# Kernel tuning notes

Measured on AMD Instinct MI355X. Metric: run time of the kernel, lower is better.

The kernel has to match this reference:

```python
import math
import jax, jax.numpy as jnp
import numpy as np

L, W, H, T, B = 12, 1024, 16, 1024, 2
CH = W // H  # per-head channels
SCALE = 1.0 / math.sqrt(math.sqrt(CH))
STD = 0.25 * math.sqrt(1.0 / W)  # init_scale * sqrt(1/width)


def setup_inputs() -> dict:
    key = jax.random.key(0)
    ks = jax.random.split(key, 8)
    x = jax.random.normal(ks[0], (B, T, W), dtype=jnp.float32)
    qkv_w = jax.random.normal(ks[1], (L, W, 3 * W), dtype=jnp.float32) * STD
    qkv_b = jnp.zeros((L, 3 * W), jnp.float32)
    proj_w = jax.random.normal(ks[2], (L, W, W), dtype=jnp.float32) * STD
    proj_b = jnp.zeros((L, W), jnp.float32)
    ln1_g = jnp.ones((L, W), jnp.float32)
    ln1_b = jnp.zeros((L, W), jnp.float32)
    ln2_g = jnp.ones((L, W), jnp.float32)
    ln2_b = jnp.zeros((L, W), jnp.float32)
    fc_w = jax.random.normal(ks[3], (L, W, 4 * W), dtype=jnp.float32) * STD
    fc_b = jnp.zeros((L, 4 * W), jnp.float32)
    fc2_w = jax.random.normal(ks[4], (L, 4 * W, W), dtype=jnp.float32) * STD
    fc2_b = jnp.zeros((L, W), jnp.float32)
    return dict(x=x, qkv_w=qkv_w, qkv_b=qkv_b, proj_w=proj_w, proj_b=proj_b,
                ln1_g=ln1_g, ln1_b=ln1_b, ln2_g=ln2_g, ln2_b=ln2_b,
                fc_w=fc_w, fc_b=fc_b, fc2_w=fc2_w, fc2_b=fc2_b)


def _ln(x, g, b, eps=1e-5):
    mu = jnp.mean(x, axis=-1, keepdims=True)
    var = jnp.mean(jnp.square(x - mu), axis=-1, keepdims=True)
    return (x - mu) * jax.lax.rsqrt(var + eps) * g + b


def _attn(h, w_qkv, b_qkv, w_p, b_p):
    bs, t, w = h.shape
    qkv = (h @ w_qkv + b_qkv).reshape(bs, t, H, 3 * CH)
    q, k, v = jnp.split(qkv, 3, axis=-1)  # each [bs, t, H, CH]
    # double-sqrt scaling as in QKVMultiheadAttention
    wts = jnp.einsum('bthc,bshc->bhts', q * SCALE, k * SCALE)
    wts = jax.nn.softmax(wts.astype(jnp.float32), axis=-1).astype(h.dtype)
    o = jnp.einsum('bhts,bshc->bthc', wts, v).reshape(bs, t, w)
    return o @ w_p + b_p


def reference(x, qkv_w, qkv_b, proj_w, proj_b, ln1_g, ln1_b, ln2_g, ln2_b,
              fc_w, fc_b, fc2_w, fc2_b):
    def step(h, p):
        wq, bq, wp, bp, g1, b1, g2, b2, wf, bf, w2, b2m = p
        h = h + _attn(_ln(h, g1, b1), wq, bq, wp, bp)
        z = _ln(h, g2, b2)
        h = h + (jax.nn.gelu(z @ wf + bf, approximate=False) @ w2 + b2m)
        return h, None
    params = (qkv_w, qkv_b, proj_w, proj_b, ln1_g, ln1_b, ln2_g, ln2_b,
              fc_w, fc_b, fc2_w, fc2_b)
    out, _ = jax.lax.scan(step, x, params)
    return out
```

## Files before the change

kernel.cpp:

```cpp
#include <hip/hip_runtime.h>
#include <hip/hip_bf16.h>
#include <math.h>

typedef __bf16 bf16;
typedef __bf16 bf16x8 __attribute__((ext_vector_type(8)));
typedef __bf16 bf16x4 __attribute__((ext_vector_type(4)));
typedef float  f32x4  __attribute__((ext_vector_type(4)));

#define DEV __device__ __forceinline__

DEV void lds_load16(const void* g, void* l) {
  __builtin_amdgcn_global_load_lds(
      (__attribute__((address_space(1))) unsigned int*)g,
      (__attribute__((address_space(3))) unsigned int*)l, 16, 0, 0);
}

DEV f32x4 mfma16(bf16x8 a, bf16x8 b, f32x4 c) {
  return __builtin_amdgcn_mfma_f32_16x16x32_bf16(a, b, c, 0, 0, 0);
}

__global__ __launch_bounds__(256) void transpose_cvt(
    const float* __restrict__ in0, bf16* __restrict__ out0, int R, int C) {
  __shared__ float t[32][33];
  size_t zo = (size_t)blockIdx.z * R * C;
  const float* in = in0 + zo;
  bf16* out = out0 + zo;
  int tx = threadIdx.x, ty = threadIdx.y;
  int c0 = blockIdx.x * 32, r0 = blockIdx.y * 32;
#pragma unroll
  for (int i = 0; i < 4; i++)
    t[ty + i * 8][tx] = in[(size_t)(r0 + ty + i * 8) * C + c0 + tx];
  __syncthreads();
#pragma unroll
  for (int i = 0; i < 4; i++)
    out[(size_t)(c0 + ty + i * 8) * R + r0 + tx] = (bf16)t[tx][ty + i * 8];
}

__global__ __launch_bounds__(256) void ln_fwd(
    const float* __restrict__ x, const float* __restrict__ gw,
    const float* __restrict__ bw, bf16* __restrict__ y,
    float* __restrict__ hout) {
  int row = blockIdx.x, tid = threadIdx.x;
  const float4 v = ((const float4*)(x + (size_t)row * 1024))[tid];
  if (hout) ((float4*)(hout + (size_t)row * 1024))[tid] = v;
  float s  = v.x + v.y + v.z + v.w;
  float s2 = v.x * v.x + v.y * v.y + v.z * v.z + v.w * v.w;
#pragma unroll
  for (int o = 1; o < 64; o <<= 1) {
    s  += __shfl_xor(s, o);
    s2 += __shfl_xor(s2, o);
  }
  __shared__ float ps[4], ps2[4];
  int wv = tid >> 6;
  if ((tid & 63) == 0) { ps[wv] = s; ps2[wv] = s2; }
  __syncthreads();
  s  = ps[0] + ps[1] + ps[2] + ps[3];
  s2 = ps2[0] + ps2[1] + ps2[2] + ps2[3];
  float mu  = s * (1.f / 1024.f);
  float var = s2 * (1.f / 1024.f) - mu * mu;
  float rs  = rsqrtf(var + 1e-5f);
  float4 gv = ((const float4*)gw)[tid];
  float4 bv = ((const float4*)bw)[tid];
  bf16x4 o4;
  o4[0] = (bf16)((v.x - mu) * rs * gv.x + bv.x);
  o4[1] = (bf16)((v.y - mu) * rs * gv.y + bv.y);
  o4[2] = (bf16)((v.z - mu) * rs * gv.z + bv.z);
  o4[3] = (bf16)((v.w - mu) * rs * gv.w + bv.w);
  *(bf16x4*)(y + (size_t)row * 1024 + tid * 4) = o4;
}

__global__ __launch_bounds__(256) void reduce_ln(
    const float* __restrict__ parts, int nparts, const float* __restrict__ bias,
    float* __restrict__ h, const float* __restrict__ gw,
    const float* __restrict__ bw, bf16* __restrict__ y) {
  const int row = blockIdx.x, tid = threadIdx.x;
  const size_t MN = (size_t)gridDim.x * 1024;
  const size_t rb = (size_t)row * 256;
  float4 s = ((const float4*)parts)[rb + tid];
  for (int p = 1; p < nparts; p++) {
    float4 v = ((const float4*)(parts + (size_t)p * MN))[rb + tid];
    s.x += v.x; s.y += v.y; s.z += v.z; s.w += v.w;
  }
  const float4 bb = ((const float4*)bias)[tid];
  float4 r = ((float4*)h)[rb + tid];
  r.x += s.x + bb.x; r.y += s.y + bb.y; r.z += s.z + bb.z; r.w += s.w + bb.w;
  ((float4*)h)[rb + tid] = r;
  if (gw == nullptr) return;
  float sm  = r.x + r.y + r.z + r.w;
  float sm2 = r.x * r.x + r.y * r.y + r.z * r.z + r.w * r.w;
#pragma unroll
  for (int o = 1; o < 64; o <<= 1) {
    sm  += __shfl_xor(sm, o);
    sm2 += __shfl_xor(sm2, o);
  }
  __shared__ float ps[4], ps2[4];
  int wv = tid >> 6;
  if ((tid & 63) == 0) { ps[wv] = sm; ps2[wv] = sm2; }
  __syncthreads();
  sm  = ps[0] + ps[1] + ps[2] + ps[3];
  sm2 = ps2[0] + ps2[1] + ps2[2] + ps2[3];
  float mu  = sm * (1.f / 1024.f);
  float var = sm2 * (1.f / 1024.f) - mu * mu;
  float rs  = rsqrtf(var + 1e-5f);
  float4 gv = ((const float4*)gw)[tid];
  float4 bv = ((const float4*)bw)[tid];
  bf16x4 o4;
  o4[0] = (bf16)((r.x - mu) * rs * gv.x + bv.x);
  o4[1] = (bf16)((r.y - mu) * rs * gv.y + bv.y);
  o4[2] = (bf16)((r.z - mu) * rs * gv.z + bv.z);
  o4[3] = (bf16)((r.w - mu) * rs * gv.w + bv.w);
  *(bf16x4*)(y + (size_t)row * 1024 + tid * 4) = o4;
}

template <int EPI>
__global__ __launch_bounds__(512, 2) void gemm8p(
    const bf16* __restrict__ A, const bf16* __restrict__ Bt,
    const float* __restrict__ bias, float* __restrict__ outf,
    bf16* __restrict__ outb, int M, int N, int K, int kcount) {
  __shared__ __align__(16) char lds[3 * 49152];
  const int tid = threadIdx.x, wv = tid >> 6, lane = tid & 63;
  const int g = lane >> 4, lr = lane & 15;
  const int wr = wv >> 2, wc = wv & 3;
  const int bn = blockIdx.x, bm = blockIdx.y;
  const int kbegin = blockIdx.z * kcount;
  const bf16* Ab = A + (size_t)bm * 128 * K + kbegin;
  const bf16* Bb = Bt + (size_t)bn * 256 * K + kbegin;
  const int nt = kcount >> 6;

  f32x4 acc[4][4] = {};

  auto stageA = [&](int t) {
    char* dst = lds + (t % 3) * 49152;
    int k0 = t * 64;
#pragma unroll
    for (int c = 0; c < 2; c++) {
      int off = c * 8192 + tid * 16;
      int row = off >> 7, cb = off & 127;
      int cbs = cb ^ ((row & 7) << 4);
      lds_load16((const char*)(Ab + (size_t)row * K + k0) + cbs, dst + off);
    }
  };
  auto stageB = [&](int t, int half) {
    char* dst = lds + (t % 3) * 49152 + 16384 + half * 16384;
    int k0 = t * 64;
#pragma unroll
    for (int c = 0; c < 2; c++) {
      int off = c * 8192 + tid * 16;
      int row = (off >> 7) + half * 128, cb = off & 127;
      int cbs = cb ^ ((row & 7) << 4);
      lds_load16((const char*)(Bb + (size_t)row * K + k0) + cbs, dst + off);
    }
  };
  auto ldA = [&](int t, int m, int kk) -> bf16x8 {
    const char* base = lds + (t % 3) * 49152;
    int row = wr * 64 + m * 16 + lr;
    int col = (kk * 64 + g * 16) ^ ((row & 7) << 4);
    return *(const bf16x8*)(base + row * 128 + col);
  };
  auto ldB = [&](int t, int n, int kk) -> bf16x8 {
    const char* base = lds + (t % 3) * 49152 + 16384;
    int row = wc * 64 + n * 16 + lr;
    int col = (kk * 64 + g * 16) ^ ((row & 7) << 4);
    return *(const bf16x8*)(base + row * 128 + col);
  };

  stageA(0); stageB(0, 0); stageB(0, 1);
  if (nt > 1) {
    stageA(1); stageB(1, 0); stageB(1, 1);
    asm volatile("s_waitcnt vmcnt(6)" ::: "memory");
  } else {
    asm volatile("s_waitcnt vmcnt(0)" ::: "memory");
  }
  __builtin_amdgcn_s_barrier();

  bf16x8 a[4][2], b[4][2];
  for (int t = 0; t < nt; ++t) {
#pragma unroll
    for (int m = 0; m < 4; m++)
#pragma unroll
      for (int kk = 0; kk < 2; kk++) a[m][kk] = ldA(t, m, kk);
#pragma unroll
    for (int n = 0; n < 2; n++)
#pragma unroll
      for (int kk = 0; kk < 2; kk++) b[n][kk] = ldB(t, n, kk);
    if (t + 2 < nt) { stageA(t + 2); stageB(t + 2, 0); }
    __builtin_amdgcn_s_barrier();
    asm volatile("s_waitcnt lgkmcnt(0)" ::: "memory");
    __builtin_amdgcn_sched_barrier(0);
    __builtin_amdgcn_s_setprio(1);
#pragma unroll
    for (int m = 0; m < 4; m++)
#pragma unroll
      for (int n = 0; n < 2; n++)
#pragma unroll
        for (int kk = 0; kk < 2; kk++)
          acc[m][n] = mfma16(a[m][kk], b[n][kk], acc[m][n]);
    __builtin_amdgcn_s_setprio(0);
    __builtin_amdgcn_s_barrier();
#pragma unroll
    for (int n = 2; n < 4; n++)
#pragma unroll
      for (int kk = 0; kk < 2; kk++) b[n][kk] = ldB(t, n, kk);
    if (t + 2 < nt) {
      stageB(t + 2, 1);
      asm volatile("s_waitcnt vmcnt(6)" ::: "memory");
    } else if (t + 1 < nt) {
      asm volatile("s_waitcnt vmcnt(0)" ::: "memory");
    }
    __builtin_amdgcn_s_barrier();
    asm volatile("s_waitcnt lgkmcnt(0)" ::: "memory");
    __builtin_amdgcn_sched_barrier(0);
    __builtin_amdgcn_s_setprio(1);
#pragma unroll
    for (int m = 0; m < 4; m++)
#pragma unroll
      for (int n = 2; n < 4; n++)
#pragma unroll
        for (int kk = 0; kk < 2; kk++)
          acc[m][n] = mfma16(a[m][kk], b[n][kk], acc[m][n]);
    __builtin_amdgcn_s_setprio(0);
    __builtin_amdgcn_s_barrier();
  }

  float* po = (EPI == 3) ? outf + (size_t)blockIdx.z * M * N : outf;
#pragma unroll
  for (int m = 0; m < 4; m++) {
#pragma unroll
    for (int n = 0; n < 4; n++) {
      int col = bn * 256 + wc * 64 + n * 16 + lr;
      float bv = (EPI == 3) ? 0.f : bias[col];
#pragma unroll
      for (int r = 0; r < 4; r++) {
        int row = bm * 128 + wr * 64 + m * 16 + g * 4 + r;
        size_t idx = (size_t)row * N + col;
        float v = acc[m][n][r] + bv;
        if (EPI == 0) {
          outb[idx] = (bf16)v;
        } else if (EPI == 2) {
          outb[idx] = (bf16)(0.5f * v * (1.f + erff(v * 0.70710678118f)));
        } else {
          po[idx] = v;
        }
      }
    }
  }
}

__global__ __launch_bounds__(256) void attn_fwd(
    const bf16* __restrict__ qkv, bf16* __restrict__ outp) {
  __shared__ __align__(16) bf16 Kls[128 * 64];
  __shared__ __align__(16) bf16 Vt[64 * 128];
  __shared__ __align__(16) bf16 Pls[4 * 16 * 128];
  const int tid = threadIdx.x, wv = tid >> 6, lane = tid & 63;
  const int g = lane >> 4, lr = lane & 15;
  const int bh = blockIdx.y, bb = bh >> 4, hh = bh & 15;
  const int q0 = blockIdx.x * 64;
  const bf16* base = qkv + (size_t)bb * 1024 * 3072;
  const int qc = hh * 192, kc = qc + 64, vc = qc + 128;

  bf16x8 aq[2];
  {
    int row = q0 + wv * 16 + lr;
#pragma unroll
    for (int kk = 0; kk < 2; kk++) {
      bf16x8 v = *(const bf16x8*)(base + (size_t)row * 3072 + qc + kk * 32 + g * 8);
#pragma unroll
      for (int j = 0; j < 8; j++) v[j] = (bf16)((float)v[j] * 0.1803368801f);
      aq[kk] = v;
    }
  }

  f32x4 o[4] = {};
  float rm[4], rl[4];
#pragma unroll
  for (int r = 0; r < 4; r++) { rm[r] = -1e30f; rl[r] = 0.f; }

  for (int s0 = 0; s0 < 1024; s0 += 128) {
#pragma unroll
    for (int c = 0; c < 4; c++) {
      int off = wv * 4096 + c * 1024 + lane * 16;
      int s = off >> 7, cb = off & 127;
      int cbs = cb ^ ((s & 7) << 4);
      lds_load16((const char*)(base + (size_t)(s0 + s) * 3072 + kc) + cbs,
                 (char*)Kls + off);
    }
#pragma unroll
    for (int it = 0; it < 2; it++) {
      int idx = it * 256 + tid;
      int s = (idx >> 3) * 2, c0i = (idx & 7) * 8;
      bf16x8 v0 = *(const bf16x8*)(base + (size_t)(s0 + s) * 3072 + vc + c0i);
      bf16x8 v1 = *(const bf16x8*)(base + (size_t)(s0 + s + 1) * 3072 + vc + c0i);
#pragma unroll
      for (int j = 0; j < 8; j++) {
        int c = c0i + j;
        unsigned int pk = (unsigned int)__builtin_bit_cast(unsigned short, v0[j]) |
                          ((unsigned int)__builtin_bit_cast(unsigned short, v1[j]) << 16);
        *(unsigned int*)((char*)Vt + c * 256 + ((s * 2) ^ ((c & 7) << 4))) = pk;
      }
    }
    __syncthreads();
    f32x4 sa[8] = {};
#pragma unroll
    for (int kk = 0; kk < 2; kk++) {
#pragma unroll
      for (int n = 0; n < 8; n++) {
        int srow = n * 16 + lr;
        int cbyte = (kk * 32 + g * 8) * 2;
        bf16x8 kb = *(const bf16x8*)((char*)Kls + srow * 128 +
                                     (cbyte ^ ((srow & 7) << 4)));
        sa[n] = mfma16(aq[kk], kb, sa[n]);
      }
    }
    float al[4];
#pragma unroll
    for (int r = 0; r < 4; r++) {
      float tm = -1e30f;
#pragma unroll
      for (int n = 0; n < 8; n++) tm = fmaxf(tm, sa[n][r]);
      tm = fmaxf(tm, __shfl_xor(tm, 1));
      tm = fmaxf(tm, __shfl_xor(tm, 2));
      tm = fmaxf(tm, __shfl_xor(tm, 4));
      tm = fmaxf(tm, __shfl_xor(tm, 8));
      float nm = fmaxf(rm[r], tm);
      al[r] = exp2f(rm[r] - nm);
      rm[r] = nm;
    }
    float psum[4] = {0.f, 0.f, 0.f, 0.f};
#pragma unroll
    for (int n = 0; n < 8; n++) {
#pragma unroll
      for (int r = 0; r < 4; r++) {
        float p = exp2f(sa[n][r] - rm[r]);
        psum[r] += p;
        int rw = g * 4 + r;
        int sb = (n * 16 + lr) * 2;
        *(bf16*)((char*)Pls + wv * 4096 + rw * 256 + (sb ^ ((rw & 7) << 4))) =
            (bf16)p;
      }
    }
#pragma unroll
    for (int r = 0; r < 4; r++) {
      psum[r] += __shfl_xor(psum[r], 1);
      psum[r] += __shfl_xor(psum[r], 2);
      psum[r] += __shfl_xor(psum[r], 4);
      psum[r] += __shfl_xor(psum[r], 8);
      rl[r] = rl[r] * al[r] + psum[r];
#pragma unroll
      for (int n = 0; n < 4; n++) o[n][r] *= al[r];
    }
    __syncthreads();
#pragma unroll
    for (int sc = 0; sc < 4; sc++) {
      int sb = (sc * 32 + g * 8) * 2;
      bf16x8 pa = *(const bf16x8*)((char*)Pls + wv * 4096 + lr * 256 +
                                   (sb ^ ((lr & 7) << 4)));
#pragma unroll
      for (int n = 0; n < 4; n++) {
        int c = n * 16 + lr;
        bf16x8 vb = *(const bf16x8*)((char*)Vt + c * 256 + (sb ^ ((c & 7) << 4)));
        o[n] = mfma16(pa, vb, o[n]);
      }
    }
    __syncthreads();
  }
#pragma unroll
  for (int n = 0; n < 4; n++)
#pragma unroll
    for (int r = 0; r < 4; r++) {
      int row = q0 + wv * 16 + g * 4 + r;
      int col = hh * 64 + n * 16 + lr;
      outp[(size_t)(bb * 1024 + row) * 1024 + col] = (bf16)(o[n][r] / rl[r]);
    }
}

extern "C" void kernel_launch(void* const* d_in, const int* in_sizes, int n_in,
                              void* d_out, int out_size, void* d_ws,
                              size_t ws_size, hipStream_t stream) {
  const float* x      = (const float*)d_in[0];
  const float* qkv_w  = (const float*)d_in[1];
  const float* qkv_b  = (const float*)d_in[2];
  const float* proj_w = (const float*)d_in[3];
  const float* proj_b = (const float*)d_in[4];
  const float* ln1_g  = (const float*)d_in[5];
  const float* ln1_b  = (const float*)d_in[6];
  const float* ln2_g  = (const float*)d_in[7];
  const float* ln2_b  = (const float*)d_in[8];
  const float* fc_w   = (const float*)d_in[9];
  const float* fc_b   = (const float*)d_in[10];
  const float* fc2_w  = (const float*)d_in[11];
  const float* fc2_b  = (const float*)d_in[12];
  float* h = (float*)d_out;

  char* ws = (char*)d_ws;
  size_t off = 0;
  auto alloc = [&](size_t bytes) -> char* {
    char* p = ws + off;
    off = (off + bytes + 255) & ~(size_t)255;
    return p;
  };
  bf16* wq_t    = (bf16*)alloc((size_t)12 * 3072 * 1024 * 2);
  bf16* wp_t    = (bf16*)alloc((size_t)12 * 1024 * 1024 * 2);
  bf16* wf_t    = (bf16*)alloc((size_t)12 * 4096 * 1024 * 2);
  bf16* w2_t    = (bf16*)alloc((size_t)12 * 1024 * 4096 * 2);
  bf16* lnbuf   = (bf16*)alloc((size_t)2048 * 1024 * 2);
  bf16* qkvbuf  = (bf16*)alloc((size_t)2048 * 3072 * 2);
  bf16* attnbuf = (bf16*)alloc((size_t)2048 * 1024 * 2);
  bf16* fcbuf   = (bf16*)alloc((size_t)2048 * 4096 * 2);
  float* partbuf = (float*)alloc((size_t)4 * 2048 * 1024 * 4);

  transpose_cvt<<<dim3(96, 32, 12), dim3(32, 8), 0, stream>>>(qkv_w, wq_t, 1024, 3072);
  transpose_cvt<<<dim3(32, 32, 12), dim3(32, 8), 0, stream>>>(proj_w, wp_t, 1024, 1024);
  transpose_cvt<<<dim3(128, 32, 12), dim3(32, 8), 0, stream>>>(fc_w, wf_t, 1024, 4096);
  transpose_cvt<<<dim3(32, 128, 12), dim3(32, 8), 0, stream>>>(fc2_w, w2_t, 4096, 1024);

  ln_fwd<<<2048, 256, 0, stream>>>(x, ln1_g, ln1_b, lnbuf, h);

  for (int l = 0; l < 12; l++) {
    const bf16* wq = wq_t + (size_t)l * 3072 * 1024;
    const bf16* wp = wp_t + (size_t)l * 1024 * 1024;
    const bf16* wf = wf_t + (size_t)l * 4096 * 1024;
    const bf16* w2 = w2_t + (size_t)l * 1024 * 4096;

    gemm8p<0><<<dim3(12, 16, 1), 512, 0, stream>>>(
        lnbuf, wq, qkv_b + (size_t)l * 3072, nullptr, qkvbuf, 2048, 3072, 1024,
        1024);
    attn_fwd<<<dim3(16, 32), 256, 0, stream>>>(qkvbuf, attnbuf);
    gemm8p<3><<<dim3(4, 16, 2), 512, 0, stream>>>(
        attnbuf, wp, nullptr, partbuf, nullptr, 2048, 1024, 1024, 512);
    reduce_ln<<<2048, 256, 0, stream>>>(partbuf, 2, proj_b + (size_t)l * 1024,
                                        h, ln2_g + (size_t)l * 1024,
                                        ln2_b + (size_t)l * 1024, lnbuf);
    gemm8p<2><<<dim3(16, 16, 1), 512, 0, stream>>>(
        lnbuf, wf, fc_b + (size_t)l * 4096, nullptr, fcbuf, 2048, 4096, 1024,
        1024);
    gemm8p<3><<<dim3(4, 16, 4), 512, 0, stream>>>(
        fcbuf, w2, nullptr, partbuf, nullptr, 2048, 1024, 4096, 1024);
    if (l < 11) {
      reduce_ln<<<2048, 256, 0, stream>>>(
          partbuf, 4, fc2_b + (size_t)l * 1024, h,
          ln1_g + (size_t)(l + 1) * 1024, ln1_b + (size_t)(l + 1) * 1024,
          lnbuf);
    } else {
      reduce_ln<<<2048, 256, 0, stream>>>(partbuf, 4,
                                          fc2_b + (size_t)l * 1024, h, nullptr,
                                          nullptr, nullptr);
    }
  }
}
```

Measured before the change: 1.884 ms.

## Double-buffer K/V tiles in attention and prefetch next tile during compute

The attention kernel now keeps two LDS buffers for K and transposed V. While the current tile is being computed, it issues the async LDS loads for the next K tile and the global loads for the next V tile into registers. The V data is written into the alternate buffer after the PV matmul. This hides global-load latency behind the score and softmax work. It also drops one block barrier per iteration and replaces another with a wave-local lgkmcnt wait, since P is per-wave. The cost is about 16KB more LDS per block and extra registers, which could lower occupancy.

```diff
diff --git a/kernel.cpp b/kernel.cpp
--- a/kernel.cpp
+++ b/kernel.cpp
@@ -248,8 +248,8 @@
 
 __global__ __launch_bounds__(256) void attn_fwd(
     const bf16* __restrict__ qkv, bf16* __restrict__ outp) {
-  __shared__ __align__(16) bf16 Kls[128 * 64];
-  __shared__ __align__(16) bf16 Vt[64 * 128];
+  __shared__ __align__(16) bf16 Kls[2][128 * 64];
+  __shared__ __align__(16) bf16 Vt[2][64 * 128];
   __shared__ __align__(16) bf16 Pls[4 * 16 * 128];
   const int tid = threadIdx.x, wv = tid >> 6, lane = tid & 63;
   const int g = lane >> 4, lr = lane & 15;
@@ -258,46 +258,53 @@
   const bf16* base = qkv + (size_t)bb * 1024 * 3072;
   const int qc = hh * 192, kc = qc + 64, vc = qc + 128;
 
-  bf16x8 aq[2];
-  {
-    int row = q0 + wv * 16 + lr;
-#pragma unroll
-    for (int kk = 0; kk < 2; kk++) {
-      bf16x8 v = *(const bf16x8*)(base + (size_t)row * 3072 + qc + kk * 32 + g * 8);
-#pragma unroll
-      for (int j = 0; j < 8; j++) v[j] = (bf16)((float)v[j] * 0.1803368801f);
-      aq[kk] = v;
-    }
-  }
-
-  f32x4 o[4] = {};
-  float rm[4], rl[4];
-#pragma unroll
-  for (int r = 0; r < 4; r++) { rm[r] = -1e30f; rl[r] = 0.f; }
-
-  for (int s0 = 0; s0 < 1024; s0 += 128) {
+  auto kstage = [&](int t, int buf) {
 #pragma unroll
     for (int c = 0; c < 4; c++) {
       int off = wv * 4096 + c * 1024 + lane * 16;
       int s = off >> 7, cb = off & 127;
       int cbs = cb ^ ((s & 7) << 4);
-      lds_load16((const char*)(base + (size_t)(s0 + s) * 3072 + kc) + cbs,
-                 (char*)Kls + off);
-    }
-#pragma unroll
-    for (int it = 0; it < 2; it++) {
-      int idx = it * 256 + tid;
-      int s = (idx >> 3) * 2, c0i = (idx & 7) * 8;
-      bf16x8 v0 = *(const bf16x8*)(base + (size_t)(s0 + s) * 3072 + vc + c0i);
-      bf16x8 v1 = *(const bf16x8*)(base + (size_t)(s0 + s + 1) * 3072 + vc + c0i);
-#pragma unroll
-      for (int j = 0; j < 8; j++) {
-        int c = c0i + j;
-        unsigned int pk = (unsigned int)__builtin_bit_cast(unsigned short, v0[j]) |
-                          ((unsigned int)__builtin_bit_cast(unsigned short, v1[j]) << 16);
-        *(unsigned int*)((char*)Vt + c * 256 + ((s * 2) ^ ((c & 7) << 4))) = pk;
-      }
-    }
+      lds_load16(
+          (const char*)(base + (size_t)(t * 128 + s) * 3072 + kc) + cbs,
+          (char*)Kls[buf] + off);
+    }
+  };
+
+  bf16x8 aq[2];
+  {
+    int row = q0 + wv * 16 + lr;
+#pragma unroll
+    for (int kk = 0; kk < 2; kk++) {
+      bf16x8 v = *(const bf16x8*)(base + (size_t)row * 3072 + qc + kk * 32 + g * 8);
+#pragma unroll
+      for (int j = 0; j < 8; j++) v[j] = (bf16)((float)v[j] * 0.1803368801f);
+      aq[kk] = v;
+    }
+  }
+
+  f32x4 o[4] = {};
+  float rm[4], rl[4];
+#pragma unroll
+  for (int r = 0; r < 4; r++) { rm[r] = -1e30f; rl[r] = 0.f; }
+
+  kstage(0, 0);
+#pragma unroll
+  for (int it = 0; it < 2; it++) {
+    int idx = it * 256 + tid;
+    int s = (idx >> 3) * 2, c0i = (idx & 7) * 8;
+    bf16x8 v0 = *(const bf16x8*)(base + (size_t)s * 3072 + vc + c0i);
+    bf16x8 v1 = *(const bf16x8*)(base + (size_t)(s + 1) * 3072 + vc + c0i);
+#pragma unroll
+    for (int j = 0; j < 8; j++) {
+      int c = c0i + j;
+      unsigned int pk = (unsigned int)__builtin_bit_cast(unsigned short, v0[j]) |
+                        ((unsigned int)__builtin_bit_cast(unsigned short, v1[j]) << 16);
+      *(unsigned int*)((char*)Vt[0] + c * 256 + ((s * 2) ^ ((c & 7) << 4))) = pk;
+    }
+  }
+
+  for (int ti = 0; ti < 8; ++ti) {
+    const int cur = ti & 1, nxt = cur ^ 1;
     __syncthreads();
     f32x4 sa[8] = {};
 #pragma unroll
@@ -306,9 +313,22 @@
       for (int n = 0; n < 8; n++) {
         int srow = n * 16 + lr;
         int cbyte = (kk * 32 + g * 8) * 2;
-        bf16x8 kb = *(const bf16x8*)((char*)Kls + srow * 128 +
+        bf16x8 kb = *(const bf16x8*)((char*)Kls[cur] + srow * 128 +
                                      (cbyte ^ ((srow & 7) << 4)));
         sa[n] = mfma16(aq[kk], kb, sa[n]);
+      }
+    }
+    bf16x8 vreg[2][2];
+    if (ti + 1 < 8) {
+      kstage(ti + 1, nxt);
+#pragma unroll
+      for (int it = 0; it < 2; it++) {
+        int idx = it * 256 + tid;
+        int s = (idx >> 3) * 2, c0i = (idx & 7) * 8;
+        vreg[it][0] = *(const bf16x8*)(
+            base + (size_t)((ti + 1) * 128 + s) * 3072 + vc + c0i);
+        vreg[it][1] = *(const bf16x8*)(
+            base + (size_t)((ti + 1) * 128 + s + 1) * 3072 + vc + c0i);
       }
     }
     float al[4];
@@ -348,7 +368,8 @@
 #pragma unroll
       for (int n = 0; n < 4; n++) o[n][r] *= al[r];
     }
-    __syncthreads();
+    asm volatile("s_waitcnt lgkmcnt(0)" ::: "memory");
+    __builtin_amdgcn_sched_barrier(0);
 #pragma unroll
     for (int sc = 0; sc < 4; sc++) {
       int sb = (sc * 32 + g * 8) * 2;
@@ -357,11 +378,28 @@
 #pragma unroll
       for (int n = 0; n < 4; n++) {
         int c = n * 16 + lr;
-        bf16x8 vb = *(const bf16x8*)((char*)Vt + c * 256 + (sb ^ ((c & 7) << 4)));
+        bf16x8 vb = *(const bf16x8*)((char*)Vt[cur] + c * 256 +
+                                     (sb ^ ((c & 7) << 4)));
         o[n] = mfma16(pa, vb, o[n]);
       }
     }
-    __syncthreads();
+    if (ti + 1 < 8) {
+#pragma unroll
+      for (int it = 0; it < 2; it++) {
+        int idx = it * 256 + tid;
+        int s = (idx >> 3) * 2, c0i = (idx & 7) * 8;
+#pragma unroll
+        for (int j = 0; j < 8; j++) {
+          int c = c0i + j;
+          unsigned int pk =
+              (unsigned int)__builtin_bit_cast(unsigned short, vreg[it][0][j]) |
+              ((unsigned int)__builtin_bit_cast(unsigned short, vreg[it][1][j])
+               << 16);
+          *(unsigned int*)((char*)Vt[nxt] + c * 256 + ((s * 2) ^ ((c & 7) << 4))) =
+              pk;
+        }
+      }
+    }
   }
 #pragma unroll
   for (int n = 0; n < 4; n++)
```

New measurement: 1.841 ms. 2.2% less time.
